# Optimization experiments

Measured on AMD Instinct MI355X. Metric: run time of the kernel, lower is better.

## Reference

```python
import jax, jax.numpy as jnp
import numpy as np

N_NODES = 100000
N_EDGES = 1200000
IN_CH = 64
HID = 16
OUT_CH = 64
EDGE_DIM = 3


def _glorot(key, shape):
    fan_in, fan_out = shape[0], shape[1]
    lim = float(np.sqrt(6.0 / (fan_in + fan_out)))
    return jax.random.uniform(key, shape, jnp.float32, -lim, lim)


def setup_inputs() -> dict:
    key = jax.random.key(0)
    ks = jax.random.split(key, 16)
    x = jax.random.normal(ks[0], (N_NODES, IN_CH), jnp.float32)
    edge_index = jax.random.randint(ks[1], (2, N_EDGES), 0, N_NODES, jnp.int64)
    edge_attr = jax.random.normal(ks[2], (N_EDGES, EDGE_DIM), jnp.float32)
    return {
        "x": x,
        "edge_index": edge_index,
        "edge_attr": edge_attr,
        # conv1: in->16
        "W1l": _glorot(ks[3], (IN_CH, HID)), "b1l": jnp.zeros((HID,), jnp.float32),
        "W1r": _glorot(ks[4], (IN_CH, HID)), "b1r": jnp.zeros((HID,), jnp.float32),
        "W1e": _glorot(ks[5], (EDGE_DIM, IN_CH)), "b1e": jnp.zeros((IN_CH,), jnp.float32),
        # conv2: 16->out
        "W2l": _glorot(ks[6], (HID, OUT_CH)), "b2l": jnp.zeros((OUT_CH,), jnp.float32),
        "W2r": _glorot(ks[7], (HID, OUT_CH)), "b2r": jnp.zeros((OUT_CH,), jnp.float32),
        "W2e": _glorot(ks[8], (EDGE_DIM, HID)), "b2e": jnp.zeros((HID,), jnp.float32),
    }


def _sage_conv(x, src, dst, edge_attr, We, be, Wl, bl, Wr, br):
    # message: neighbor feature + projected edge attribute (edge_dim-aware SAGE)
    msg = x[src] + edge_attr @ We + be                       # [E, C_in]
    agg = jax.ops.segment_sum(msg, dst, num_segments=N_NODES)  # [N, C_in]
    deg = jax.ops.segment_sum(jnp.ones((msg.shape[0],), msg.dtype), dst,
                              num_segments=N_NODES)
    agg = agg / jnp.maximum(deg, 1.0)[:, None]               # mean aggregation
    return agg @ Wl + bl + x @ Wr + br                       # neighbor + self paths


def reference(x, edge_index, edge_attr,
              W1l, b1l, W1r, b1r, W1e, b1e,
              W2l, b2l, W2r, b2r, W2e, b2e):
    src, dst = edge_index[0], edge_index[1]
    h = jax.nn.relu(_sage_conv(x, src, dst, edge_attr, W1e, b1e, W1l, b1l, W1r, b1r))
    # F.dropout(training=self.training): eval mode -> identity
    out = _sage_conv(h, src, dst, edge_attr, W2e, b2e, W2l, b2l, W2r, b2r)
    return out
```

## Files before the change

kernel.cpp:

```cpp
#include <hip/hip_runtime.h>
#include <hip/hip_bf16.h>
#include <stdint.h>

#define N_NODES 100000
#define N_EDGES 1200000
#define IN_CH 64
#define HID 16
#define OUT_CH 64

#define BN 100
#define NB 1000
#define BCAP 2048
#define CAP 2048

#define F_TPB 512
#define KY_BLOCKS ((N_NODES * 2 + F_TPB - 1) / F_TPB)
#define SC_EPB 2048
#define SC_EPT (SC_EPB / F_TPB)
#define SC_BLOCKS ((N_EDGES + SC_EPB - 1) / SC_EPB)
#define F_GROUPS 196

typedef __hip_bfloat16 bf16;

__device__ __forceinline__ float b2f(bf16 v) { return __bfloat162float(v); }
__device__ __forceinline__ float lo_f(uint32_t p) { return __uint_as_float(p << 16); }
__device__ __forceinline__ float hi_f(uint32_t p) { return __uint_as_float(p & 0xffff0000u); }
__device__ __forceinline__ uint16_t f2bb(float v) {
    bf16 h = __float2bfloat16(v);
    return *reinterpret_cast<uint16_t*>(&h);
}

__device__ __forceinline__ float loadf(const void* p, size_t i, int bf) {
    return bf ? b2f(((const bf16*)p)[i]) : ((const float*)p)[i];
}
__device__ __forceinline__ uint32_t bfbits(const void* p, size_t i, int bf) {
    if (bf) return ((const uint16_t*)p)[i];
    return f2bb(((const float*)p)[i]);
}
__device__ __forceinline__ int ld_dst(const int* p, int j, int i64) {
    if (i64) return ((const int2*)p)[(size_t)N_EDGES + j].x;
    return p[(size_t)N_EDGES + j];
}
__device__ __forceinline__ int ld_src(const int* p, int j, int i64) {
    if (i64) return ((const int2*)p)[j].x;
    return p[j];
}

__device__ __forceinline__ int detect_bf(const void* x) {
    const uint16_t* u = (const uint16_t*)x;
    int cnt = 0;
    for (int i = 0; i < 64; ++i) {
        int e = (u[i] >> 7) & 0xff;
        cnt += (e >= 100 && e <= 140);
    }
    return cnt >= 50;
}
__device__ __forceinline__ int detect_i64(const int* ei) {
    const uint32_t* w = (const uint32_t*)ei;
    int z = 0;
    for (int i = 1; i < 64; i += 2) z += (w[i] == 0u);
    return z >= 16;
}

__global__ void __launch_bounds__(F_TPB) k_fused(const void* __restrict__ x,
                                                 const int* __restrict__ ei,
                                                 const void* __restrict__ ea,
                                                 const void* __restrict__ W1l,
                                                 const void* __restrict__ W1r,
                                                 const void* __restrict__ b1l,
                                                 const void* __restrict__ b1r,
                                                 const void* __restrict__ W1e,
                                                 const void* __restrict__ b1e,
                                                 bf16* __restrict__ y,
                                                 bf16* __restrict__ zh,
                                                 float* __restrict__ wc,
                                                 int* __restrict__ gcnt,
                                                 uint2* __restrict__ slots,
                                                 uint16_t* __restrict__ ea2v) {
    __shared__ __align__(16) char smem[36608];
    __shared__ int wsum[8];
    __shared__ int s_flags;
    int t = threadIdx.x;
    int g = blockIdx.x / 5, r = blockIdx.x % 5;
    if (t == 0) s_flags = detect_bf(x) | (detect_i64(ei) << 1);

    if (r < 2) {
        int kyid = g * 2 + r;
        if (kyid >= KY_BLOCKS) return;
        float* w = (float*)smem;
        float* bz = (float*)(smem + 8192);
        __syncthreads();
        int bf = s_flags & 1;
        for (int i = t; i < IN_CH * 32; i += F_TPB) {
            int k = i >> 5, cc = i & 31;
            w[i] = (cc < 16) ? loadf(W1l, k * HID + cc, bf)
                             : loadf(W1r, k * HID + (cc - 16), bf);
        }
        if (t < HID) bz[t] = loadf(b1l, t, bf) + loadf(b1r, t, bf);
        __syncthreads();
        if (kyid == 0 && t < HID) {
            int j = t;
            float s0 = 0.f, s1 = 0.f, s2 = 0.f, s3 = 0.f;
            for (int k = 0; k < IN_CH; ++k) {
                float wl = w[k * 32 + j];
                s0 += loadf(W1e, k, bf) * wl;
                s1 += loadf(W1e, IN_CH + k, bf) * wl;
                s2 += loadf(W1e, 2 * IN_CH + k, bf) * wl;
                s3 += loadf(b1e, k, bf) * wl;
            }
            wc[j] = s0;
            wc[HID + j] = s1;
            wc[2 * HID + j] = s2;
            wc[3 * HID + j] = s3;
        }
        int tid = kyid * F_TPB + t;
        int row = tid >> 1;
        if (row >= N_NODES) return;
        int half = tid & 1, cs = half * 16;
        float acc[16];
#pragma unroll
        for (int j = 0; j < 16; ++j) acc[j] = 0.f;
        if (bf) {
            const uint4* xr = (const uint4*)((const uint16_t*)x + (size_t)row * IN_CH);
            uint4 q[8];
#pragma unroll
            for (int i = 0; i < 8; ++i) q[i] = xr[i];
            const uint32_t* qq = (const uint32_t*)q;
#pragma unroll
            for (int k2 = 0; k2 < 32; ++k2) {
                uint32_t u = qq[k2];
                float x0 = lo_f(u), x1 = hi_f(u);
                const float* w0 = &w[(2 * k2) * 32 + cs];
                const float* w1 = w0 + 32;
#pragma unroll
                for (int j = 0; j < 16; ++j) acc[j] += x0 * w0[j] + x1 * w1[j];
            }
        } else {
            const float4* xr = (const float4*)((const float*)x + (size_t)row * IN_CH);
#pragma unroll
            for (int c = 0; c < 4; ++c) {
                float4 f[4];
#pragma unroll
                for (int i = 0; i < 4; ++i) f[i] = xr[c * 4 + i];
                const float* ff = (const float*)f;
#pragma unroll
                for (int kk = 0; kk < 16; ++kk) {
                    float xk = ff[kk];
                    const float* wr = &w[(c * 16 + kk) * 32 + cs];
#pragma unroll
                    for (int j = 0; j < 16; ++j) acc[j] += xk * wr[j];
                }
            }
        }
        if (half) {
#pragma unroll
            for (int j = 0; j < 16; ++j) acc[j] += bz[j];
        }
        uint32_t pk[8];
#pragma unroll
        for (int j2 = 0; j2 < 8; ++j2)
            pk[j2] = (uint32_t)f2bb(acc[2 * j2]) | ((uint32_t)f2bb(acc[2 * j2 + 1]) << 16);
        bf16* dst = half ? (zh + (size_t)row * HID) : (y + (size_t)row * HID);
        uint4* d4 = (uint4*)dst;
        d4[0] = make_uint4(pk[0], pk[1], pk[2], pk[3]);
        d4[1] = make_uint4(pk[4], pk[5], pk[6], pk[7]);
        return;
    }

    int scid = g * 3 + (r - 2);
    if (scid >= SC_BLOCKS) return;
    uint2* lval = (uint2*)smem;
    int* lhist = (int*)(smem + 16384);
    int* lscan = (int*)(smem + 20384);
    int* ldelta = (int*)(smem + 24384);
    uint16_t* lea = (uint16_t*)(smem + 28384);
    uint16_t* lbid = (uint16_t*)(smem + 32480);
    for (int i = t; i < NB; i += F_TPB) lhist[i] = 0;
    __syncthreads();
    int bf = s_flags & 1, i64 = (s_flags >> 1) & 1;
    int base = scid * SC_EPB;
    uint32_t rb[SC_EPT], srcv[SC_EPT], ea01v[SC_EPT], ea2r[SC_EPT];
#pragma unroll
    for (int i = 0; i < SC_EPT; ++i) {
        int e = base + i * F_TPB + t;
        rb[i] = 0xFFFFFFFFu;
        if (e < N_EDGES) {
            uint32_t d = (uint32_t)ld_dst(ei, e, i64);
            srcv[i] = (uint32_t)ld_src(ei, e, i64);
            ea01v[i] = bfbits(ea, (size_t)e * 3, bf) |
                       (bfbits(ea, (size_t)e * 3 + 1, bf) << 16);
            ea2r[i] = bfbits(ea, (size_t)e * 3 + 2, bf);
            uint32_t b = d / BN;
            uint32_t dl = d - b * BN;
            uint32_t rr = (uint32_t)atomicAdd(&lhist[b], 1);
            rb[i] = (b << 19) | (dl << 12) | rr;
        }
    }
    __syncthreads();
    int b0 = 2 * t, b1 = 2 * t + 1;
    int cnt0 = (b0 < NB) ? lhist[b0] : 0;
    int cnt1 = (b1 < NB) ? lhist[b1] : 0;
    int s_local = cnt0 + cnt1;
    int incl = s_local;
    int lane = t & 63;
#pragma unroll
    for (int d = 1; d < 64; d <<= 1) {
        int v = __shfl_up(incl, d);
        if (lane >= d) incl += v;
    }
    int w = t >> 6;
    if (lane == 63) wsum[w] = incl;
    __syncthreads();
    int wbase = 0, nst = 0;
#pragma unroll
    for (int i = 0; i < 8; ++i) {
        int v = wsum[i];
        wbase += (i < w) ? v : 0;
        nst += v;
    }
    int run = wbase + incl - s_local;
    if (b0 < NB) {
        lscan[b0] = run;
        if (cnt0) ldelta[b0] = b0 * BCAP + atomicAdd(&gcnt[b0], cnt0) - run;
    }
    run += cnt0;
    if (b1 < NB) {
        lscan[b1] = run;
        if (cnt1) ldelta[b1] = b1 * BCAP + atomicAdd(&gcnt[b1], cnt1) - run;
    }
    __syncthreads();
#pragma unroll
    for (int i = 0; i < SC_EPT; ++i) {
        if (rb[i] == 0xFFFFFFFFu) continue;
        uint32_t b = rb[i] >> 19;
        uint32_t dl = (rb[i] >> 12) & 0x7Fu;
        uint32_t rr = rb[i] & 0xFFFu;
        int lp = lscan[b] + (int)rr;
        lval[lp] = make_uint2(srcv[i] | (dl << 17), ea01v[i]);
        lea[lp] = (uint16_t)ea2r[i];
        lbid[lp] = (uint16_t)b;
    }
    __syncthreads();
    for (int p = t; p < nst; p += F_TPB) {
        int b = lbid[p];
        int gp = ldelta[b] + p;
        slots[gp] = lval[p];
        ea2v[gp] = lea[p];
    }
}

#define SORT_CHUNK(nst)                                                        \
    {                                                                          \
        for (int i_ = t; i_ < (nst); i_ += 256)                                \
            atomicAdd(&hist[su[i_].x >> 17], 1);                               \
        __syncthreads();                                                       \
        if (t < 128) sbuf[t] = (t < BN) ? hist[t] : 0;                         \
        __syncthreads();                                                       \
        for (int off_ = 1; off_ < 128; off_ <<= 1) {                           \
            int v_ = 0;                                                        \
            if (t < 128 && t >= off_) v_ = sbuf[t - off_];                     \
            __syncthreads();                                                   \
            if (t < 128) sbuf[t] += v_;                                        \
            __syncthreads();                                                   \
        }                                                                      \
        if (t < BN) {                                                          \
            int ex_ = sbuf[t] - hist[t];                                       \
            noff[t] = ex_;                                                     \
            cur[t] = ex_;                                                      \
        }                                                                      \
        __syncthreads();                                                       \
        for (int i_ = t; i_ < (nst); i_ += 256) {                              \
            int r_ = atomicAdd(&cur[su[i_].x >> 17], 1);                       \
            sidx[r_] = (uint16_t)i_;                                           \
        }                                                                      \
        __syncthreads();                                                       \
    }

__global__ void __launch_bounds__(256) k_agg1(const uint2* __restrict__ slots,
                                              const uint16_t* __restrict__ ea2v,
                                              const int* __restrict__ gcnt,
                                              const bf16* __restrict__ y,
                                              const float* __restrict__ wc,
                                              bf16* __restrict__ zh,
                                              float* __restrict__ sa,
                                              uint32_t* __restrict__ ssrc,
                                              int* __restrict__ nof2) {
    __shared__ uint2 su[CAP];
    __shared__ uint16_t ea2s[CAP];
    __shared__ uint16_t sidx[CAP];
    __shared__ int hist[BN], noff[BN], cur[BN], sbuf[128];
    __shared__ float swc[64];
    int t = threadIdx.x;
    if (t < 64) swc[t] = wc[t];
    int b = blockIdx.x;
    int n = gcnt[b];
    if (n > CAP) n = CAP;
    const uint2* sp = slots + (size_t)b * BCAP;
    const uint16_t* ep = ea2v + (size_t)b * BCAP;
    int dl = t >> 1, half = t & 1, cs = half * 8;
    float acc[8] = {0.f, 0.f, 0.f, 0.f, 0.f, 0.f, 0.f, 0.f};
    float a0 = 0.f, a1 = 0.f, a2 = 0.f, degT = 0.f;

    for (int i_ = t; i_ < BN; i_ += 256) hist[i_] = 0;
    for (int i_ = t; i_ < n; i_ += 256) {
        su[i_] = sp[i_];
        ea2s[i_] = ep[i_];
    }
    __syncthreads();
    SORT_CHUNK(n)
    for (int p = t; p < n; p += 256) ssrc[(size_t)b * BCAP + p] = su[sidx[p]].x;
    if (t < BN) nof2[b * 128 + t] = noff[t];
    if (dl < BN) {
        int kb = noff[dl];
        int ke = (dl == BN - 1) ? n : noff[dl + 1];
        int k = kb;
        for (; k + 3 < ke; k += 4) {
            int i0 = sidx[k], i1 = sidx[k + 1], i2 = sidx[k + 2], i3 = sidx[k + 3];
            uint2 s0 = su[i0], s1 = su[i1], s2 = su[i2], s3 = su[i3];
            uint4 q0 = *(const uint4*)(y + (size_t)(s0.x & 0x1FFFFu) * HID + cs);
            uint4 q1 = *(const uint4*)(y + (size_t)(s1.x & 0x1FFFFu) * HID + cs);
            uint4 q2 = *(const uint4*)(y + (size_t)(s2.x & 0x1FFFFu) * HID + cs);
            uint4 q3 = *(const uint4*)(y + (size_t)(s3.x & 0x1FFFFu) * HID + cs);
            acc[0] += lo_f(q0.x) + lo_f(q1.x) + lo_f(q2.x) + lo_f(q3.x);
            acc[1] += hi_f(q0.x) + hi_f(q1.x) + hi_f(q2.x) + hi_f(q3.x);
            acc[2] += lo_f(q0.y) + lo_f(q1.y) + lo_f(q2.y) + lo_f(q3.y);
            acc[3] += hi_f(q0.y) + hi_f(q1.y) + hi_f(q2.y) + hi_f(q3.y);
            acc[4] += lo_f(q0.z) + lo_f(q1.z) + lo_f(q2.z) + lo_f(q3.z);
            acc[5] += hi_f(q0.z) + hi_f(q1.z) + hi_f(q2.z) + hi_f(q3.z);
            acc[6] += lo_f(q0.w) + lo_f(q1.w) + lo_f(q2.w) + lo_f(q3.w);
            acc[7] += hi_f(q0.w) + hi_f(q1.w) + hi_f(q2.w) + hi_f(q3.w);
            if (half == 0) {
                a0 += lo_f(s0.y) + lo_f(s1.y) + lo_f(s2.y) + lo_f(s3.y);
                a1 += hi_f(s0.y) + hi_f(s1.y) + hi_f(s2.y) + hi_f(s3.y);
                a2 += __uint_as_float((uint32_t)ea2s[i0] << 16) +
                      __uint_as_float((uint32_t)ea2s[i1] << 16) +
                      __uint_as_float((uint32_t)ea2s[i2] << 16) +
                      __uint_as_float((uint32_t)ea2s[i3] << 16);
            }
        }
        for (; k < ke; ++k) {
            int i0 = sidx[k];
            uint2 s0 = su[i0];
            uint4 q0 = *(const uint4*)(y + (size_t)(s0.x & 0x1FFFFu) * HID + cs);
            acc[0] += lo_f(q0.x); acc[1] += hi_f(q0.x);
            acc[2] += lo_f(q0.y); acc[3] += hi_f(q0.y);
            acc[4] += lo_f(q0.z); acc[5] += hi_f(q0.z);
            acc[6] += lo_f(q0.w); acc[7] += hi_f(q0.w);
            if (half == 0) {
                a0 += lo_f(s0.y);
                a1 += hi_f(s0.y);
                a2 += __uint_as_float((uint32_t)ea2s[i0] << 16);
            }
        }
        degT = (float)hist[dl];
    }
    if (dl < BN) {
        a0 += __shfl_xor(a0, 1);
        a1 += __shfl_xor(a1, 1);
        a2 += __shfl_xor(a2, 1);
        size_t i = (size_t)b * BN + dl;
        float inv = 1.0f / fmaxf(degT, 1.0f);
        uint4 zq = *(const uint4*)(zh + i * HID + cs);
        float zf[8] = {lo_f(zq.x), hi_f(zq.x), lo_f(zq.y), hi_f(zq.y),
                       lo_f(zq.z), hi_f(zq.z), lo_f(zq.w), hi_f(zq.w)};
        uint32_t pk[4];
#pragma unroll
        for (int j = 0; j < 4; ++j) {
            float t0 = (acc[2 * j] + a0 * swc[cs + 2 * j] + a1 * swc[16 + cs + 2 * j] +
                        a2 * swc[32 + cs + 2 * j] + degT * swc[48 + cs + 2 * j]) * inv;
            float t1 = (acc[2 * j + 1] + a0 * swc[cs + 2 * j + 1] + a1 * swc[17 + cs + 2 * j] +
                        a2 * swc[33 + cs + 2 * j] + degT * swc[49 + cs + 2 * j]) * inv;
            float h0 = fmaxf(t0 + zf[2 * j], 0.f);
            float h1 = fmaxf(t1 + zf[2 * j + 1], 0.f);
            pk[j] = (uint32_t)f2bb(h0) | ((uint32_t)f2bb(h1) << 16);
        }
        *(uint4*)(zh + i * HID + cs) = make_uint4(pk[0], pk[1], pk[2], pk[3]);
        if (half == 0) {
            sa[i * 3 + 0] = a0;
            sa[i * 3 + 1] = a1;
            sa[i * 3 + 2] = a2;
        }
    }
}

__global__ void __launch_bounds__(256) k_agg2(const void* __restrict__ x,
                                              const uint32_t* __restrict__ ssrc,
                                              const int* __restrict__ nof2,
                                              const int* __restrict__ gcnt,
                                              const bf16* __restrict__ zh,
                                              const float* __restrict__ sa,
                                              const void* __restrict__ W2l,
                                              const void* __restrict__ b2l,
                                              const void* __restrict__ W2r,
                                              const void* __restrict__ b2r,
                                              const void* __restrict__ W2e,
                                              const void* __restrict__ b2e,
                                              void* __restrict__ out) {
    __shared__ uint32_t ss[CAP];
    __shared__ int snoff[BN];
    __shared__ float facc[BN * HID];
    __shared__ bf16 hl[BN * HID];
    __shared__ float w2l[HID * OUT_CH];
    __shared__ float w2r[HID * OUT_CH];
    __shared__ float swe[3 * HID];
    __shared__ float sbe[HID];
    __shared__ float sbb[OUT_CH];
    __shared__ int s_bf;
    int t = threadIdx.x;
    if (t == 0) s_bf = detect_bf(x);
    __syncthreads();
    int bf = s_bf;
    for (int i = t; i < HID * OUT_CH; i += 256) {
        w2l[i] = loadf(W2l, i, bf);
        w2r[i] = loadf(W2r, i, bf);
    }
    if (t < 3 * HID) swe[t] = loadf(W2e, t, bf);
    if (t < HID) sbe[t] = loadf(b2e, t, bf);
    if (t < OUT_CH) sbb[t] = loadf(b2l, t, bf) + loadf(b2r, t, bf);
    int b = blockIdx.x;
    int n = gcnt[b];
    if (n > CAP) n = CAP;
    for (int i = t; i < n; i += 256) ss[i] = ssrc[(size_t)b * BCAP + i];
    if (t < BN) snoff[t] = nof2[b * 128 + t];
    __syncthreads();
    int dl = t >> 1, half = t & 1, cs = half * 8;
    float acc[8] = {0.f, 0.f, 0.f, 0.f, 0.f, 0.f, 0.f, 0.f};
    float degT = 0.f;
    if (dl < BN) {
        int kb = snoff[dl];
        int ke = (dl == BN - 1) ? n : snoff[dl + 1];
        degT = (float)(ke - kb);
        int k = kb;
        for (; k + 3 < ke; k += 4) {
            uint32_t s0 = ss[k], s1 = ss[k + 1], s2 = ss[k + 2], s3 = ss[k + 3];
            uint4 q0 = *(const uint4*)(zh + (size_t)(s0 & 0x1FFFFu) * HID + cs);
            uint4 q1 = *(const uint4*)(zh + (size_t)(s1 & 0x1FFFFu) * HID + cs);
            uint4 q2 = *(const uint4*)(zh + (size_t)(s2 & 0x1FFFFu) * HID + cs);
            uint4 q3 = *(const uint4*)(zh + (size_t)(s3 & 0x1FFFFu) * HID + cs);
            acc[0] += lo_f(q0.x) + lo_f(q1.x) + lo_f(q2.x) + lo_f(q3.x);
            acc[1] += hi_f(q0.x) + hi_f(q1.x) + hi_f(q2.x) + hi_f(q3.x);
            acc[2] += lo_f(q0.y) + lo_f(q1.y) + lo_f(q2.y) + lo_f(q3.y);
            acc[3] += hi_f(q0.y) + hi_f(q1.y) + hi_f(q2.y) + hi_f(q3.y);
            acc[4] += lo_f(q0.z) + lo_f(q1.z) + lo_f(q2.z) + lo_f(q3.z);
            acc[5] += hi_f(q0.z) + hi_f(q1.z) + hi_f(q2.z) + hi_f(q3.z);
            acc[6] += lo_f(q0.w) + lo_f(q1.w) + lo_f(q2.w) + lo_f(q3.w);
            acc[7] += hi_f(q0.w) + hi_f(q1.w) + hi_f(q2.w) + hi_f(q3.w);
        }
        for (; k < ke; ++k) {
            uint32_t s0 = ss[k];
            uint4 q0 = *(const uint4*)(zh + (size_t)(s0 & 0x1FFFFu) * HID + cs);
            acc[0] += lo_f(q0.x); acc[1] += hi_f(q0.x);
            acc[2] += lo_f(q0.y); acc[3] += hi_f(q0.y);
            acc[4] += lo_f(q0.z); acc[5] += hi_f(q0.z);
            acc[6] += lo_f(q0.w); acc[7] += hi_f(q0.w);
        }
    }
    if (dl < BN) {
        size_t i = (size_t)b * BN + dl;
        float inv = 1.0f / fmaxf(degT, 1.0f);
        float a0 = sa[i * 3 + 0], a1 = sa[i * 3 + 1], a2 = sa[i * 3 + 2];
        float4 f0, f1;
        float* fo = (float*)&f0;
        float* f1o = (float*)&f1;
#pragma unroll
        for (int j = 0; j < 4; ++j) {
            fo[j] = (acc[j] + a0 * swe[cs + j] + a1 * swe[16 + cs + j] +
                     a2 * swe[32 + cs + j] + degT * sbe[cs + j]) * inv;
            f1o[j] = (acc[4 + j] + a0 * swe[cs + 4 + j] + a1 * swe[16 + cs + 4 + j] +
                      a2 * swe[32 + cs + 4 + j] + degT * sbe[cs + 4 + j]) * inv;
        }
        *(float4*)&facc[dl * HID + cs] = f0;
        *(float4*)&facc[dl * HID + cs + 4] = f1;
        *(uint4*)&hl[dl * HID + cs] = *(const uint4*)(zh + i * HID + cs);
    }
    __syncthreads();
    for (int idx = t; idx < BN * OUT_CH; idx += 256) {
        int dli = idx >> 6, j = idx & 63;
        size_t i = (size_t)b * BN + dli;
        float o = sbb[j];
#pragma unroll
        for (int cc = 0; cc < HID; ++cc)
            o += facc[dli * HID + cc] * w2l[cc * OUT_CH + j] +
                 b2f(hl[dli * HID + cc]) * w2r[cc * OUT_CH + j];
        if (bf)
            ((bf16*)out)[i * OUT_CH + j] = __float2bfloat16(o);
        else
            ((float*)out)[i * OUT_CH + j] = o;
    }
}

extern "C" void kernel_launch(void* const* d_in, const int* in_sizes, int n_in,
                              void* d_out, int out_size, void* d_ws, size_t ws_size,
                              hipStream_t stream) {
    const void* x   = d_in[0];
    const int*  ei  = (const int*)d_in[1];
    const void* ea  = d_in[2];
    const void* W1l = d_in[3];
    const void* b1l = d_in[4];
    const void* W1r = d_in[5];
    const void* b1r = d_in[6];
    const void* W1e = d_in[7];
    const void* b1e = d_in[8];
    const void* W2l = d_in[9];
    const void* b2l = d_in[10];
    const void* W2r = d_in[11];
    const void* b2r = d_in[12];
    const void* W2e = d_in[13];
    const void* b2e = d_in[14];

    const size_t N16 = (size_t)N_NODES * HID;
    char* p = (char*)d_ws;
    uint2*    slots = (uint2*)p;    p += (size_t)NB * BCAP * sizeof(uint2);
    uint16_t* ea2v  = (uint16_t*)p; p += (size_t)NB * BCAP * sizeof(uint16_t);
    uint32_t* ssrc  = (uint32_t*)p; p += (size_t)NB * BCAP * sizeof(uint32_t);
    int*      nof2  = (int*)p;      p += (size_t)NB * 128 * sizeof(int);
    bf16*     y     = (bf16*)p;     p += N16 * sizeof(bf16);
    bf16*     zh    = (bf16*)p;     p += N16 * sizeof(bf16);
    float*    sa    = (float*)p;    p += (size_t)3 * N_NODES * sizeof(float);
    int*      gcnt  = (int*)p;      p += NB * sizeof(int);
    float*    wc    = (float*)p;    p += 64 * sizeof(float);

    hipMemsetAsync(gcnt, 0, NB * sizeof(int), stream);
    k_fused<<<F_GROUPS * 5, F_TPB, 0, stream>>>(x, ei, ea, W1l, W1r, b1l, b1r, W1e, b1e,
                                                y, zh, wc, gcnt, slots, ea2v);
    k_agg1<<<NB, 256, 0, stream>>>(slots, ea2v, gcnt, y, wc, zh, sa, ssrc, nof2);
    k_agg2<<<NB, 256, 0, stream>>>(x, ssrc, nof2, gcnt, zh, sa, W2l, b2l, W2r, b2r,
                                   W2e, b2e, d_out);
}
```

Measured before the change: 194.0 us.

## Make every fused block run both projection and scatter phases in alternating order

The first kernel used to split its blocks into specialised roles, two of every five doing the node projection and three doing the edge bucket scatter, across 980 blocks. Now 512 blocks each handle one projection tile of 196 rows and one scatter tile of 2344 edges. Half the blocks run projection first and the other half run scatter first, so memory-bound and compute-bound phases overlap across the device. This balances work per block and removes the block-role imbalance, but it lengthens each block, adds barriers and raises shared memory per block, which may lower occupancy.

```diff
diff --git a/kernel.cpp b/kernel.cpp
--- a/kernel.cpp
+++ b/kernel.cpp
@@ -14,11 +14,17 @@
 #define CAP 2048
 
 #define F_TPB 512
-#define KY_BLOCKS ((N_NODES * 2 + F_TPB - 1) / F_TPB)
-#define SC_EPB 2048
-#define SC_EPT (SC_EPB / F_TPB)
-#define SC_BLOCKS ((N_EDGES + SC_EPB - 1) / SC_EPB)
-#define F_GROUPS 196
+#define F_BLOCKS 512
+#define SC_EPB 2344
+#define SC_EPT 5
+#define KY_RPB 196
+#define O_LVAL 0
+#define O_LHIST 18752
+#define O_LSCAN 22752
+#define O_LDELTA 26752
+#define O_LEA 30752
+#define O_LBID 35440
+#define SMEM_BYTES 40128
 
 typedef __hip_bfloat16 bf16;
 
@@ -60,6 +66,187 @@
     int z = 0;
     for (int i = 1; i < 64; i += 2) z += (w[i] == 0u);
     return z >= 16;
+}
+
+__device__ __forceinline__ void sc_phase(int scid, int bf, int i64,
+                                         const int* __restrict__ ei,
+                                         const void* __restrict__ ea,
+                                         int* __restrict__ gcnt,
+                                         uint2* __restrict__ slots,
+                                         uint16_t* __restrict__ ea2v,
+                                         char* smem, int* wsum) {
+    uint2* lval = (uint2*)(smem + O_LVAL);
+    int* lhist = (int*)(smem + O_LHIST);
+    int* lscan = (int*)(smem + O_LSCAN);
+    int* ldelta = (int*)(smem + O_LDELTA);
+    uint16_t* lea = (uint16_t*)(smem + O_LEA);
+    uint16_t* lbid = (uint16_t*)(smem + O_LBID);
+    int t = threadIdx.x;
+    for (int i = t; i < NB; i += F_TPB) lhist[i] = 0;
+    __syncthreads();
+    int base = scid * SC_EPB;
+    uint32_t rb[SC_EPT], srcv[SC_EPT], ea01v[SC_EPT], ea2r[SC_EPT];
+#pragma unroll
+    for (int i = 0; i < SC_EPT; ++i) {
+        int le = i * F_TPB + t;
+        rb[i] = 0xFFFFFFFFu;
+        if (le < SC_EPB && base + le < N_EDGES) {
+            int e = base + le;
+            uint32_t d = (uint32_t)ld_dst(ei, e, i64);
+            srcv[i] = (uint32_t)ld_src(ei, e, i64);
+            ea01v[i] = bfbits(ea, (size_t)e * 3, bf) |
+                       (bfbits(ea, (size_t)e * 3 + 1, bf) << 16);
+            ea2r[i] = bfbits(ea, (size_t)e * 3 + 2, bf);
+            uint32_t b = d / BN;
+            uint32_t dl = d - b * BN;
+            uint32_t rr = (uint32_t)atomicAdd(&lhist[b], 1);
+            rb[i] = (b << 19) | (dl << 12) | rr;
+        }
+    }
+    __syncthreads();
+    int b0 = 2 * t, b1 = 2 * t + 1;
+    int cnt0 = (b0 < NB) ? lhist[b0] : 0;
+    int cnt1 = (b1 < NB) ? lhist[b1] : 0;
+    int s_local = cnt0 + cnt1;
+    int incl = s_local;
+    int lane = t & 63;
+#pragma unroll
+    for (int d = 1; d < 64; d <<= 1) {
+        int v = __shfl_up(incl, d);
+        if (lane >= d) incl += v;
+    }
+    int w = t >> 6;
+    if (lane == 63) wsum[w] = incl;
+    __syncthreads();
+    int wbase = 0, nst = 0;
+#pragma unroll
+    for (int i = 0; i < 8; ++i) {
+        int v = wsum[i];
+        wbase += (i < w) ? v : 0;
+        nst += v;
+    }
+    int run = wbase + incl - s_local;
+    if (b0 < NB) {
+        lscan[b0] = run;
+        if (cnt0) ldelta[b0] = b0 * BCAP + atomicAdd(&gcnt[b0], cnt0) - run;
+    }
+    run += cnt0;
+    if (b1 < NB) {
+        lscan[b1] = run;
+        if (cnt1) ldelta[b1] = b1 * BCAP + atomicAdd(&gcnt[b1], cnt1) - run;
+    }
+    __syncthreads();
+#pragma unroll
+    for (int i = 0; i < SC_EPT; ++i) {
+        if (rb[i] == 0xFFFFFFFFu) continue;
+        uint32_t b = rb[i] >> 19;
+        uint32_t dl = (rb[i] >> 12) & 0x7Fu;
+        uint32_t rr = rb[i] & 0xFFFu;
+        int lp = lscan[b] + (int)rr;
+        lval[lp] = make_uint2(srcv[i] | (dl << 17), ea01v[i]);
+        lea[lp] = (uint16_t)ea2r[i];
+        lbid[lp] = (uint16_t)b;
+    }
+    __syncthreads();
+    for (int p = t; p < nst; p += F_TPB) {
+        int b = lbid[p];
+        int gp = ldelta[b] + p;
+        slots[gp] = lval[p];
+        ea2v[gp] = lea[p];
+    }
+    __syncthreads();
+}
+
+__device__ __forceinline__ void ky_phase(int bid, int bf,
+                                         const void* __restrict__ x,
+                                         const void* __restrict__ W1l,
+                                         const void* __restrict__ W1r,
+                                         const void* __restrict__ b1l,
+                                         const void* __restrict__ b1r,
+                                         const void* __restrict__ W1e,
+                                         const void* __restrict__ b1e,
+                                         bf16* __restrict__ y,
+                                         bf16* __restrict__ zh,
+                                         float* __restrict__ wc,
+                                         char* smem) {
+    float* w = (float*)smem;
+    float* bz = (float*)(smem + 8192);
+    int t = threadIdx.x;
+    __syncthreads();
+    for (int i = t; i < IN_CH * 32; i += F_TPB) {
+        int k = i >> 5, cc = i & 31;
+        w[i] = (cc < 16) ? loadf(W1l, k * HID + cc, bf)
+                         : loadf(W1r, k * HID + (cc - 16), bf);
+    }
+    if (t < HID) bz[t] = loadf(b1l, t, bf) + loadf(b1r, t, bf);
+    __syncthreads();
+    if (bid == 0 && t < HID) {
+        int j = t;
+        float s0 = 0.f, s1 = 0.f, s2 = 0.f, s3 = 0.f;
+        for (int k = 0; k < IN_CH; ++k) {
+            float wl = w[k * 32 + j];
+            s0 += loadf(W1e, k, bf) * wl;
+            s1 += loadf(W1e, IN_CH + k, bf) * wl;
+            s2 += loadf(W1e, 2 * IN_CH + k, bf) * wl;
+            s3 += loadf(b1e, k, bf) * wl;
+        }
+        wc[j] = s0;
+        wc[HID + j] = s1;
+        wc[2 * HID + j] = s2;
+        wc[3 * HID + j] = s3;
+    }
+    int row = bid * KY_RPB + (t >> 1);
+    if (t < KY_RPB * 2 && row < N_NODES) {
+        int half = t & 1, cs = half * 16;
+        float acc[16];
+#pragma unroll
+        for (int j = 0; j < 16; ++j) acc[j] = 0.f;
+        if (bf) {
+            const uint4* xr = (const uint4*)((const uint16_t*)x + (size_t)row * IN_CH);
+            uint4 q[8];
+#pragma unroll
+            for (int i = 0; i < 8; ++i) q[i] = xr[i];
+            const uint32_t* qq = (const uint32_t*)q;
+#pragma unroll
+            for (int k2 = 0; k2 < 32; ++k2) {
+                uint32_t u = qq[k2];
+                float x0 = lo_f(u), x1 = hi_f(u);
+                const float* w0 = &w[(2 * k2) * 32 + cs];
+                const float* w1 = w0 + 32;
+#pragma unroll
+                for (int j = 0; j < 16; ++j) acc[j] += x0 * w0[j] + x1 * w1[j];
+            }
+        } else {
+            const float4* xr = (const float4*)((const float*)x + (size_t)row * IN_CH);
+#pragma unroll
+            for (int c = 0; c < 4; ++c) {
+                float4 f[4];
+#pragma unroll
+                for (int i = 0; i < 4; ++i) f[i] = xr[c * 4 + i];
+                const float* ff = (const float*)f;
+#pragma unroll
+                for (int kk = 0; kk < 16; ++kk) {
+                    float xk = ff[kk];
+                    const float* wr = &w[(c * 16 + kk) * 32 + cs];
+#pragma unroll
+                    for (int j = 0; j < 16; ++j) acc[j] += xk * wr[j];
+                }
+            }
+        }
+        if (half) {
+#pragma unroll
+            for (int j = 0; j < 16; ++j) acc[j] += bz[j];
+        }
+        uint32_t pk[8];
+#pragma unroll
+        for (int j2 = 0; j2 < 8; ++j2)
+            pk[j2] = (uint32_t)f2bb(acc[2 * j2]) | ((uint32_t)f2bb(acc[2 * j2 + 1]) << 16);
+        bf16* dst = half ? (zh + (size_t)row * HID) : (y + (size_t)row * HID);
+        uint4* d4 = (uint4*)dst;
+        d4[0] = make_uint4(pk[0], pk[1], pk[2], pk[3]);
+        d4[1] = make_uint4(pk[4], pk[5], pk[6], pk[7]);
+    }
+    __syncthreads();
 }
 
 __global__ void __launch_bounds__(F_TPB) k_fused(const void* __restrict__ x,
@@ -77,175 +264,19 @@
                                                  int* __restrict__ gcnt,
                                                  uint2* __restrict__ slots,
                                                  uint16_t* __restrict__ ea2v) {
-    __shared__ __align__(16) char smem[36608];
+    __shared__ __align__(16) char smem[SMEM_BYTES];
     __shared__ int wsum[8];
     __shared__ int s_flags;
-    int t = threadIdx.x;
-    int g = blockIdx.x / 5, r = blockIdx.x % 5;
-    if (t == 0) s_flags = detect_bf(x) | (detect_i64(ei) << 1);
-
-    if (r < 2) {
-        int kyid = g * 2 + r;
-        if (kyid >= KY_BLOCKS) return;
-        float* w = (float*)smem;
-        float* bz = (float*)(smem + 8192);
-        __syncthreads();
-        int bf = s_flags & 1;
-        for (int i = t; i < IN_CH * 32; i += F_TPB) {
-            int k = i >> 5, cc = i & 31;
-            w[i] = (cc < 16) ? loadf(W1l, k * HID + cc, bf)
-                             : loadf(W1r, k * HID + (cc - 16), bf);
-        }
-        if (t < HID) bz[t] = loadf(b1l, t, bf) + loadf(b1r, t, bf);
-        __syncthreads();
-        if (kyid == 0 && t < HID) {
-            int j = t;
-            float s0 = 0.f, s1 = 0.f, s2 = 0.f, s3 = 0.f;
-            for (int k = 0; k < IN_CH; ++k) {
-                float wl = w[k * 32 + j];
-                s0 += loadf(W1e, k, bf) * wl;
-                s1 += loadf(W1e, IN_CH + k, bf) * wl;
-                s2 += loadf(W1e, 2 * IN_CH + k, bf) * wl;
-                s3 += loadf(b1e, k, bf) * wl;
-            }
-            wc[j] = s0;
-            wc[HID + j] = s1;
-            wc[2 * HID + j] = s2;
-            wc[3 * HID + j] = s3;
-        }
-        int tid = kyid * F_TPB + t;
-        int row = tid >> 1;
-        if (row >= N_NODES) return;
-        int half = tid & 1, cs = half * 16;
-        float acc[16];
-#pragma unroll
-        for (int j = 0; j < 16; ++j) acc[j] = 0.f;
-        if (bf) {
-            const uint4* xr = (const uint4*)((const uint16_t*)x + (size_t)row * IN_CH);
-            uint4 q[8];
-#pragma unroll
-            for (int i = 0; i < 8; ++i) q[i] = xr[i];
-            const uint32_t* qq = (const uint32_t*)q;
-#pragma unroll
-            for (int k2 = 0; k2 < 32; ++k2) {
-                uint32_t u = qq[k2];
-                float x0 = lo_f(u), x1 = hi_f(u);
-                const float* w0 = &w[(2 * k2) * 32 + cs];
-                const float* w1 = w0 + 32;
-#pragma unroll
-                for (int j = 0; j < 16; ++j) acc[j] += x0 * w0[j] + x1 * w1[j];
-            }
-        } else {
-            const float4* xr = (const float4*)((const float*)x + (size_t)row * IN_CH);
-#pragma unroll
-            for (int c = 0; c < 4; ++c) {
-                float4 f[4];
-#pragma unroll
-                for (int i = 0; i < 4; ++i) f[i] = xr[c * 4 + i];
-                const float* ff = (const float*)f;
-#pragma unroll
-                for (int kk = 0; kk < 16; ++kk) {
-                    float xk = ff[kk];
-                    const float* wr = &w[(c * 16 + kk) * 32 + cs];
-#pragma unroll
-                    for (int j = 0; j < 16; ++j) acc[j] += xk * wr[j];
-                }
-            }
-        }
-        if (half) {
-#pragma unroll
-            for (int j = 0; j < 16; ++j) acc[j] += bz[j];
-        }
-        uint32_t pk[8];
-#pragma unroll
-        for (int j2 = 0; j2 < 8; ++j2)
-            pk[j2] = (uint32_t)f2bb(acc[2 * j2]) | ((uint32_t)f2bb(acc[2 * j2 + 1]) << 16);
-        bf16* dst = half ? (zh + (size_t)row * HID) : (y + (size_t)row * HID);
-        uint4* d4 = (uint4*)dst;
-        d4[0] = make_uint4(pk[0], pk[1], pk[2], pk[3]);
-        d4[1] = make_uint4(pk[4], pk[5], pk[6], pk[7]);
-        return;
-    }
-
-    int scid = g * 3 + (r - 2);
-    if (scid >= SC_BLOCKS) return;
-    uint2* lval = (uint2*)smem;
-    int* lhist = (int*)(smem + 16384);
-    int* lscan = (int*)(smem + 20384);
-    int* ldelta = (int*)(smem + 24384);
-    uint16_t* lea = (uint16_t*)(smem + 28384);
-    uint16_t* lbid = (uint16_t*)(smem + 32480);
-    for (int i = t; i < NB; i += F_TPB) lhist[i] = 0;
+    if (threadIdx.x == 0) s_flags = detect_bf(x) | (detect_i64(ei) << 1);
     __syncthreads();
     int bf = s_flags & 1, i64 = (s_flags >> 1) & 1;
-    int base = scid * SC_EPB;
-    uint32_t rb[SC_EPT], srcv[SC_EPT], ea01v[SC_EPT], ea2r[SC_EPT];
-#pragma unroll
-    for (int i = 0; i < SC_EPT; ++i) {
-        int e = base + i * F_TPB + t;
-        rb[i] = 0xFFFFFFFFu;
-        if (e < N_EDGES) {
-            uint32_t d = (uint32_t)ld_dst(ei, e, i64);
-            srcv[i] = (uint32_t)ld_src(ei, e, i64);
-            ea01v[i] = bfbits(ea, (size_t)e * 3, bf) |
-                       (bfbits(ea, (size_t)e * 3 + 1, bf) << 16);
-            ea2r[i] = bfbits(ea, (size_t)e * 3 + 2, bf);
-            uint32_t b = d / BN;
-            uint32_t dl = d - b * BN;
-            uint32_t rr = (uint32_t)atomicAdd(&lhist[b], 1);
-            rb[i] = (b << 19) | (dl << 12) | rr;
-        }
-    }
-    __syncthreads();
-    int b0 = 2 * t, b1 = 2 * t + 1;
-    int cnt0 = (b0 < NB) ? lhist[b0] : 0;
-    int cnt1 = (b1 < NB) ? lhist[b1] : 0;
-    int s_local = cnt0 + cnt1;
-    int incl = s_local;
-    int lane = t & 63;
-#pragma unroll
-    for (int d = 1; d < 64; d <<= 1) {
-        int v = __shfl_up(incl, d);
-        if (lane >= d) incl += v;
-    }
-    int w = t >> 6;
-    if (lane == 63) wsum[w] = incl;
-    __syncthreads();
-    int wbase = 0, nst = 0;
-#pragma unroll
-    for (int i = 0; i < 8; ++i) {
-        int v = wsum[i];
-        wbase += (i < w) ? v : 0;
-        nst += v;
-    }
-    int run = wbase + incl - s_local;
-    if (b0 < NB) {
-        lscan[b0] = run;
-        if (cnt0) ldelta[b0] = b0 * BCAP + atomicAdd(&gcnt[b0], cnt0) - run;
-    }
-    run += cnt0;
-    if (b1 < NB) {
-        lscan[b1] = run;
-        if (cnt1) ldelta[b1] = b1 * BCAP + atomicAdd(&gcnt[b1], cnt1) - run;
-    }
-    __syncthreads();
-#pragma unroll
-    for (int i = 0; i < SC_EPT; ++i) {
-        if (rb[i] == 0xFFFFFFFFu) continue;
-        uint32_t b = rb[i] >> 19;
-        uint32_t dl = (rb[i] >> 12) & 0x7Fu;
-        uint32_t rr = rb[i] & 0xFFFu;
-        int lp = lscan[b] + (int)rr;
-        lval[lp] = make_uint2(srcv[i] | (dl << 17), ea01v[i]);
-        lea[lp] = (uint16_t)ea2r[i];
-        lbid[lp] = (uint16_t)b;
-    }
-    __syncthreads();
-    for (int p = t; p < nst; p += F_TPB) {
-        int b = lbid[p];
-        int gp = ldelta[b] + p;
-        slots[gp] = lval[p];
-        ea2v[gp] = lea[p];
+    int bid = blockIdx.x;
+    if (bid < F_BLOCKS / 2) {
+        ky_phase(bid, bf, x, W1l, W1r, b1l, b1r, W1e, b1e, y, zh, wc, smem);
+        sc_phase(bid, bf, i64, ei, ea, gcnt, slots, ea2v, smem, wsum);
+    } else {
+        sc_phase(bid, bf, i64, ei, ea, gcnt, slots, ea2v, smem, wsum);
+        ky_phase(bid, bf, x, W1l, W1r, b1l, b1r, W1e, b1e, y, zh, wc, smem);
     }
 }
 
@@ -521,8 +552,8 @@
     float*    wc    = (float*)p;    p += 64 * sizeof(float);
 
     hipMemsetAsync(gcnt, 0, NB * sizeof(int), stream);
-    k_fused<<<F_GROUPS * 5, F_TPB, 0, stream>>>(x, ei, ea, W1l, W1r, b1l, b1r, W1e, b1e,
-                                                y, zh, wc, gcnt, slots, ea2v);
+    k_fused<<<F_BLOCKS, F_TPB, 0, stream>>>(x, ei, ea, W1l, W1r, b1l, b1r, W1e, b1e,
+                                            y, zh, wc, gcnt, slots, ea2v);
     k_agg1<<<NB, 256, 0, stream>>>(slots, ea2v, gcnt, y, wc, zh, sa, ssrc, nof2);
     k_agg2<<<NB, 256, 0, stream>>>(x, ssrc, nof2, gcnt, zh, sa, W2l, b2l, W2r, b2r,
                                    W2e, b2e, d_out);
```

Result: slower. 210.7 us (+8.6%).
